# Kernel tuning notes

Hardware: AMD Instinct MI355X
Metric: run time of the kernel (lower is better)

Reference implementation:

```python
import jax, jax.numpy as jnp
import numpy as np

N = 100000       # nodes
E = 3200000      # edges (avg degree 32)
NFEAT = 512
NHID = 256
NCLASS = 64
K = 10
ALPHA = 0.1


def setup_inputs() -> dict:
    key = jax.random.key(0)
    ks = jax.random.split(key, 6)
    x = jax.random.normal(ks[0], (N, NFEAT), dtype=jnp.float32)
    edge_index = jax.random.randint(ks[1], (2, E), 0, N)
    W1 = jax.random.normal(ks[2], (NFEAT, NHID), dtype=jnp.float32) / np.float32(np.sqrt(NFEAT))
    b1 = jnp.zeros((NHID,), jnp.float32)
    W2 = jax.random.normal(ks[3], (NHID, NCLASS), dtype=jnp.float32) / np.float32(np.sqrt(NHID))
    b2 = jnp.zeros((NCLASS,), jnp.float32)
    # PPR init of the K+1 GPR coefficients: alpha*(1-alpha)^k, last = (1-alpha)^K
    kk = jnp.arange(K + 1, dtype=jnp.float32)
    temp = (ALPHA * (1.0 - ALPHA) ** kk).astype(jnp.float32)
    temp = temp.at[-1].set(np.float32((1.0 - ALPHA) ** K))
    return {"x": x, "edge_index": edge_index, "W1": W1, "b1": b1, "W2": W2, "b2": b2, "temp": temp}


def reference(x, edge_index, W1, b1, W2, b2, temp):
    # MLP (dropout is identity in eval mode)
    h = jax.nn.relu(x @ W1 + b1)          # [N, NHID]
    h = h @ W2 + b2                        # [N, NCLASS]

    # gcn_norm with self-loops: D^-1/2 (A+I) D^-1/2
    row, col = edge_index[0], edge_index[1]
    loops = jnp.arange(N, dtype=row.dtype)
    row = jnp.concatenate([row, loops])
    col = jnp.concatenate([col, loops])
    w = jnp.ones(row.shape[0], h.dtype)
    deg = jax.ops.segment_sum(w, col, num_segments=N)
    dis = jnp.where(deg > 0, jax.lax.rsqrt(deg), 0.0)
    norm = dis[row] * w * dis[col]         # [E+N]

    # K-hop GPR propagation: hidden = sum_k temp[k] * A_hat^k h
    hidden = h * temp[0]
    for k in range(K):
        h = jax.ops.segment_sum(norm[:, None] * h[row], col, num_segments=N)
        hidden = hidden + temp[k + 1] * h
    return jax.nn.log_softmax(hidden, axis=1)
```

## Files before the change

kernel.cpp:

```cpp
#include <hip/hip_runtime.h>
#include <math.h>

#define NFEAT 512
#define NHID  256
#define NCLS  64
#define KHOP  10
#define LDSTRIDE 56

typedef __attribute__((ext_vector_type(8))) short short8;
typedef __attribute__((ext_vector_type(4))) float f32x4;

__device__ __forceinline__ unsigned short f2bf(float f) {
    unsigned u = __float_as_uint(f);
    u += 0x7FFFu + ((u >> 16) & 1u);
    return (unsigned short)(u >> 16);
}
__device__ __forceinline__ float bf2f(unsigned short h) {
    return __uint_as_float((unsigned)h << 16);
}

__global__ __launch_bounds__(256) void cast_kernel(const float* __restrict__ src,
                                                   unsigned short* __restrict__ dst, long n)
{
    long i = (long)blockIdx.x * 1024 + (long)threadIdx.x * 4;
    if (i + 3 < n) {
        float4 v = *(const float4*)(src + i);
        dst[i+0] = f2bf(v.x); dst[i+1] = f2bf(v.y);
        dst[i+2] = f2bf(v.z); dst[i+3] = f2bf(v.w);
    } else {
        for (int j = 0; j < 4 && i + j < n; j++) dst[i+j] = f2bf(src[i+j]);
    }
}

__global__ __launch_bounds__(256) void castT_kernel(const float* __restrict__ src,
                                                    unsigned short* __restrict__ dst,
                                                    int K, int N)
{
    int i = blockIdx.x * 256 + threadIdx.x;
    if (i < K * N) {
        int k = i / N, n = i % N;
        dst[(long)n * K + k] = f2bf(src[i]);
    }
}

__global__ __launch_bounds__(256) void mfma_gemm1(
    const unsigned short* __restrict__ A, const unsigned short* __restrict__ BT,
    const float* __restrict__ bias, unsigned short* __restrict__ C, int M)
{
    __shared__ unsigned short As[128 * LDSTRIDE];
    __shared__ unsigned short Bs[128 * LDSTRIDE];
    const int tid = threadIdx.x;
    const int wave = tid >> 6, lane = tid & 63;
    const int quad = lane >> 4, l16 = lane & 15;
    const int wm = wave >> 1, wn = wave & 1;
    const int m0 = blockIdx.x * 128, n0 = blockIdx.y * 128;

    f32x4 acc[4][4] = {};
    const int srow = tid >> 2;
    const int schunk = (tid & 3) * 8;

    for (int k0 = 0; k0 < NFEAT; k0 += 32) {
        #pragma unroll
        for (int i = 0; i < 2; i++) {
            int r = srow + i * 64;
            int rg = m0 + r;
            short8 v = {};
            if (rg < M) v = *(const short8*)(A + (long)rg * NFEAT + k0 + schunk);
            *(short8*)(As + r * LDSTRIDE + schunk) = v;
        }
        #pragma unroll
        for (int i = 0; i < 2; i++) {
            int r = srow + i * 64;
            short8 v = *(const short8*)(BT + (long)(n0 + r) * NFEAT + k0 + schunk);
            *(short8*)(Bs + r * LDSTRIDE + schunk) = v;
        }
        __syncthreads();
        short8 af[4], bfr[4];
        #pragma unroll
        for (int mi = 0; mi < 4; mi++)
            af[mi] = *(const short8*)(As + (wm*64 + mi*16 + l16) * LDSTRIDE + quad*8);
        #pragma unroll
        for (int nj = 0; nj < 4; nj++)
            bfr[nj] = *(const short8*)(Bs + (wn*64 + nj*16 + l16) * LDSTRIDE + quad*8);
        #pragma unroll
        for (int mi = 0; mi < 4; mi++)
            #pragma unroll
            for (int nj = 0; nj < 4; nj++)
                acc[mi][nj] = __builtin_amdgcn_mfma_f32_16x16x32_bf16(af[mi], bfr[nj], acc[mi][nj], 0, 0, 0);
        __syncthreads();
    }

    #pragma unroll
    for (int mi = 0; mi < 4; mi++)
        #pragma unroll
        for (int r = 0; r < 4; r++) {
            int row = m0 + wm*64 + mi*16 + quad*4 + r;
            if (row >= M) continue;
            #pragma unroll
            for (int nj = 0; nj < 4; nj++) {
                int col = n0 + wn*64 + nj*16 + l16;
                float v = acc[mi][nj][r] + bias[col];
                C[(long)row * NHID + col] = f2bf(fmaxf(v, 0.f));
            }
        }
}

__global__ __launch_bounds__(256) void mfma_gemm2(
    const unsigned short* __restrict__ A, const unsigned short* __restrict__ BT,
    const float* __restrict__ bias, unsigned short* __restrict__ S,
    float* __restrict__ hidden, const float* __restrict__ temp,
    const float* __restrict__ dis, int M)
{
    __shared__ unsigned short As[128 * LDSTRIDE];
    __shared__ unsigned short Bs[64 * LDSTRIDE];
    const int tid = threadIdx.x;
    const int wave = tid >> 6, lane = tid & 63;
    const int quad = lane >> 4, l16 = lane & 15;
    const int m0 = blockIdx.x * 128;
    const float t0 = temp[0];

    f32x4 acc[2][4] = {};
    const int srow = tid >> 2;
    const int schunk = (tid & 3) * 8;

    for (int k0 = 0; k0 < NHID; k0 += 32) {
        #pragma unroll
        for (int i = 0; i < 2; i++) {
            int r = srow + i * 64;
            int rg = m0 + r;
            short8 v = {};
            if (rg < M) v = *(const short8*)(A + (long)rg * NHID + k0 + schunk);
            *(short8*)(As + r * LDSTRIDE + schunk) = v;
        }
        {
            short8 v = *(const short8*)(BT + (long)srow * NHID + k0 + schunk);
            *(short8*)(Bs + srow * LDSTRIDE + schunk) = v;
        }
        __syncthreads();
        short8 af[2], bfr[4];
        #pragma unroll
        for (int mi = 0; mi < 2; mi++)
            af[mi] = *(const short8*)(As + (wave*32 + mi*16 + l16) * LDSTRIDE + quad*8);
        #pragma unroll
        for (int nj = 0; nj < 4; nj++)
            bfr[nj] = *(const short8*)(Bs + (nj*16 + l16) * LDSTRIDE + quad*8);
        #pragma unroll
        for (int mi = 0; mi < 2; mi++)
            #pragma unroll
            for (int nj = 0; nj < 4; nj++)
                acc[mi][nj] = __builtin_amdgcn_mfma_f32_16x16x32_bf16(af[mi], bfr[nj], acc[mi][nj], 0, 0, 0);
        __syncthreads();
    }

    #pragma unroll
    for (int mi = 0; mi < 2; mi++)
        #pragma unroll
        for (int r = 0; r < 4; r++) {
            int row = m0 + wave*32 + mi*16 + quad*4 + r;
            if (row >= M) continue;
            float dr = dis[row];
            #pragma unroll
            for (int nj = 0; nj < 4; nj++) {
                int col = nj*16 + l16;
                float v = acc[mi][nj][r] + bias[col];
                long idx = (long)row * NCLS + col;
                S[idx] = f2bf(dr * v);
                hidden[idx] = t0 * v;
            }
        }
}

__global__ void count_kernel(const int* __restrict__ ei, int E, int* __restrict__ cnt)
{
    int e = blockIdx.x * blockDim.x + threadIdx.x;
    if (e < E) atomicAdd(&cnt[ei[E + e]], 1);
}

__global__ void dis_kernel(const int* __restrict__ cnt, float* __restrict__ dis, int Nn)
{
    int v = blockIdx.x * blockDim.x + threadIdx.x;
    if (v < Nn) dis[v] = rsqrtf((float)(cnt[v] + 1));
}

__global__ __launch_bounds__(256) void bsum_kernel(const int* __restrict__ cnt, int n,
                                                   int* __restrict__ bsum)
{
    __shared__ int ws[4];
    int i = blockIdx.x * 256 + threadIdx.x;
    int v = (i < n) ? ((cnt[i] + 7) & ~7) : 0;
    #pragma unroll
    for (int off = 1; off < 64; off <<= 1) v += __shfl_xor(v, off);
    if ((threadIdx.x & 63) == 0) ws[threadIdx.x >> 6] = v;
    __syncthreads();
    if (threadIdx.x == 0) bsum[blockIdx.x] = ws[0] + ws[1] + ws[2] + ws[3];
}

__global__ __launch_bounds__(512) void bscan_kernel(int* __restrict__ bsum, int nb)
{
    __shared__ int buf[512];
    int i = threadIdx.x;
    int v = (i < nb) ? bsum[i] : 0;
    buf[i] = v;
    __syncthreads();
    for (int off = 1; off < 512; off <<= 1) {
        int t = (i >= off) ? buf[i - off] : 0;
        __syncthreads();
        buf[i] += t;
        __syncthreads();
    }
    if (i < nb) bsum[i] = buf[i] - v;
}

__global__ __launch_bounds__(256) void pscan_kernel(const int* __restrict__ cnt, int n,
                                                    const int* __restrict__ bsum,
                                                    int* __restrict__ ptr)
{
    __shared__ int buf[256];
    int i = blockIdx.x * 256 + threadIdx.x;
    int v = (i < n) ? ((cnt[i] + 7) & ~7) : 0;
    buf[threadIdx.x] = v;
    __syncthreads();
    for (int off = 1; off < 256; off <<= 1) {
        int t = (threadIdx.x >= off) ? buf[threadIdx.x - off] : 0;
        __syncthreads();
        buf[threadIdx.x] += t;
        __syncthreads();
    }
    if (i < n) ptr[i] = bsum[blockIdx.x] + buf[threadIdx.x] - v;
    if (i == n - 1) ptr[n] = bsum[blockIdx.x] + buf[threadIdx.x];
}

__global__ void fill_kernel(const int* __restrict__ ei, int E,
                            const int* __restrict__ ptr, int* __restrict__ fill,
                            int* __restrict__ adj)
{
    int e = blockIdx.x * blockDim.x + threadIdx.x;
    if (e >= E) return;
    int r = ei[e];
    int c = ei[E + e];
    int pos = atomicAdd(&fill[c], 1);
    adj[ptr[c] + pos] = r;
}

__global__ void padfill_kernel(const int* __restrict__ cnt, const int* __restrict__ ptr,
                               int* __restrict__ adj, int Nn)
{
    int v = blockIdx.x * 256 + threadIdx.x;
    if (v >= Nn) return;
    int b = ptr[v] + cnt[v], e = ptr[v + 1];
    for (int i = b; i < e; i++) adj[i] = Nn;
}

__global__ void zdum_kernel(unsigned short* __restrict__ sA,
                            unsigned short* __restrict__ sB, int Nn)
{
    int i = threadIdx.x;
    if (i < 64) sA[(long)Nn * NCLS + i] = 0;
    else        sB[(long)Nn * NCLS + (i - 64)] = 0;
}

__global__ __launch_bounds__(256) void prop_kernel(
    const unsigned short* __restrict__ sin, unsigned short* __restrict__ sout,
    float* __restrict__ hidden,
    const int* __restrict__ ptr, const int* __restrict__ adj,
    const float* __restrict__ dis, const float* __restrict__ temp, int k, int Nn)
{
    const int wave = threadIdx.x >> 6, lane = threadIdx.x & 63;
    const int v = blockIdx.x * 4 + wave;
    if (v >= Nn) return;

    const int beg = ptr[v], end = ptr[v + 1];
    const float d = dis[v];
    float acc = bf2f(sin[v * NCLS + lane]);

    for (int e = beg; e < end; e += 8) {
        int4 u0 = *(const int4*)(adj + e);
        int4 u1 = *(const int4*)(adj + e + 4);
        float a0 = bf2f(sin[u0.x * NCLS + lane]);
        float a1 = bf2f(sin[u0.y * NCLS + lane]);
        float a2 = bf2f(sin[u0.z * NCLS + lane]);
        float a3 = bf2f(sin[u0.w * NCLS + lane]);
        float a4 = bf2f(sin[u1.x * NCLS + lane]);
        float a5 = bf2f(sin[u1.y * NCLS + lane]);
        float a6 = bf2f(sin[u1.z * NCLS + lane]);
        float a7 = bf2f(sin[u1.w * NCLS + lane]);
        acc += ((a0 + a1) + (a2 + a3)) + ((a4 + a5) + (a6 + a7));
    }

    int idx = v * NCLS + lane;
    float h = d * acc;
    hidden[idx] += temp[k + 1] * h;
    sout[idx] = f2bf(d * h);
}

__global__ __launch_bounds__(256) void lsm_kernel(const float* __restrict__ hidden,
                                                  float* __restrict__ out, int Nn)
{
    const int wave = threadIdx.x >> 6, lane = threadIdx.x & 63;
    const int v = blockIdx.x * 4 + wave;
    if (v >= Nn) return;
    float x = hidden[(long)v * NCLS + lane];
    float m = x;
    #pragma unroll
    for (int off = 32; off > 0; off >>= 1) m = fmaxf(m, __shfl_xor(m, off));
    float s = __expf(x - m);
    #pragma unroll
    for (int off = 32; off > 0; off >>= 1) s += __shfl_xor(s, off);
    out[(long)v * NCLS + lane] = x - m - logf(s);
}

extern "C" void kernel_launch(void* const* d_in, const int* in_sizes, int n_in,
                              void* d_out, int out_size, void* d_ws, size_t ws_size,
                              hipStream_t stream)
{
    const float* x    = (const float*)d_in[0];
    const int*   ei   = (const int*)  d_in[1];
    const float* W1   = (const float*)d_in[2];
    const float* b1   = (const float*)d_in[3];
    const float* W2   = (const float*)d_in[4];
    const float* b2   = (const float*)d_in[5];
    const float* temp = (const float*)d_in[6];

    const int Nn = in_sizes[0] / NFEAT;
    const int E  = in_sizes[1] / 2;

    char* ws = (char*)d_ws;
    size_t off = 0;
    auto alloc = [&](size_t bytes) { size_t o = off; off += (bytes + 255) & ~255ull; return o; };

    size_t r0 = alloc((size_t)Nn * NFEAT * 2);
    size_t hmid_off = alloc((size_t)Nn * NHID * 2);
    size_t w1t_off  = alloc((size_t)NFEAT * NHID * 2);
    size_t w2t_off  = alloc((size_t)NHID * NCLS * 2);
    size_t cnt_off  = alloc((size_t)Nn * 4);
    size_t fill_off = alloc((size_t)Nn * 4);
    size_t dis_off  = alloc((size_t)Nn * 4);
    size_t ptr_off  = alloc((size_t)(Nn + 1) * 4);
    size_t bsum_off = alloc(((size_t)Nn / 256 + 2) * 4);

    unsigned short* x_bf = (unsigned short*)(ws + r0);
    unsigned short* hmid = (unsigned short*)(ws + hmid_off);
    unsigned short* W1T  = (unsigned short*)(ws + w1t_off);
    unsigned short* W2T  = (unsigned short*)(ws + w2t_off);
    int*   cnt   = (int*)  (ws + cnt_off);
    int*   fillb = (int*)  (ws + fill_off);
    float* dis   = (float*)(ws + dis_off);
    int*   ptr   = (int*)  (ws + ptr_off);
    int*   bsum  = (int*)  (ws + bsum_off);

    size_t Epad = (size_t)E + 8ull * Nn;
    int*            adj    = (int*)           (ws + r0);
    unsigned short* sA     = (unsigned short*)(ws + r0 + Epad * 4);
    unsigned short* sB     = (unsigned short*)(ws + r0 + Epad * 4 + (size_t)(Nn + 1) * NCLS * 2);
    float*          hidden = (float*)         (ws + r0 + Epad * 4 + (size_t)(Nn + 1) * NCLS * 4);

    cast_kernel<<<(int)(((long)Nn * NFEAT + 1023) / 1024), 256, 0, stream>>>(x, x_bf, (long)Nn * NFEAT);
    castT_kernel<<<(NFEAT * NHID + 255) / 256, 256, 0, stream>>>(W1, W1T, NFEAT, NHID);
    castT_kernel<<<(NHID * NCLS + 255) / 256, 256, 0, stream>>>(W2, W2T, NHID, NCLS);

    {
        dim3 g((Nn + 127) / 128, NHID / 128);
        mfma_gemm1<<<g, 256, 0, stream>>>(x_bf, W1T, b1, hmid, Nn);
    }

    hipMemsetAsync(cnt,   0, (size_t)Nn * 4, stream);
    hipMemsetAsync(fillb, 0, (size_t)Nn * 4, stream);
    count_kernel<<<(E + 255) / 256, 256, 0, stream>>>(ei, E, cnt);
    dis_kernel<<<(Nn + 255) / 256, 256, 0, stream>>>(cnt, dis, Nn);
    int nb = (Nn + 255) / 256;
    bsum_kernel<<<nb, 256, 0, stream>>>(cnt, Nn, bsum);
    bscan_kernel<<<1, 512, 0, stream>>>(bsum, nb);
    pscan_kernel<<<nb, 256, 0, stream>>>(cnt, Nn, bsum, ptr);
    fill_kernel<<<(E + 255) / 256, 256, 0, stream>>>(ei, E, ptr, fillb, adj);
    padfill_kernel<<<(Nn + 255) / 256, 256, 0, stream>>>(cnt, ptr, adj, Nn);
    zdum_kernel<<<1, 128, 0, stream>>>(sA, sB, Nn);

    mfma_gemm2<<<(Nn + 127) / 128, 256, 0, stream>>>(hmid, W2T, b2, sA, hidden, temp, dis, Nn);

    int pg = (Nn + 3) / 4;
    for (int k = 0; k < KHOP; k++) {
        const unsigned short* sin = (k & 1) ? sB : sA;
        unsigned short*       so  = (k & 1) ? sA : sB;
        prop_kernel<<<pg, 256, 0, stream>>>(sin, so, hidden, ptr, adj, dis, temp, k, Nn);
    }

    lsm_kernel<<<pg, 256, 0, stream>>>(hidden, (float*)d_out, Nn);
}
```

Measured before the change: 1.414 ms.

## Bucket edges before CSR fill and split neighbor gathers across half-waves

CSR construction now does a two-pass bucketed scatter: edges are first grouped by 256-node destination buckets into a temporary buffer, then a per-bucket kernel fills the adjacency list, so the scattered writes stay local. The propagation kernel has each half-wave handle 8 neighbors, loading packed bf16 pairs as 32-bit words, and combines the two halves with a shuffle. Degree padding rises from 8 to 16 to match. This aims to cut random-write cost in CSR build and raise gather parallelism per node, but adds an extra pass, extra memory traffic and more padding entries for low-degree nodes.

```diff
diff --git a/kernel.cpp b/kernel.cpp
--- a/kernel.cpp
+++ b/kernel.cpp
@@ -6,6 +6,7 @@
 #define NCLS  64
 #define KHOP  10
 #define LDSTRIDE 56
+#define DEGPAD 16
 
 typedef __attribute__((ext_vector_type(8))) short short8;
 typedef __attribute__((ext_vector_type(4))) float f32x4;
@@ -18,6 +19,8 @@
 __device__ __forceinline__ float bf2f(unsigned short h) {
     return __uint_as_float((unsigned)h << 16);
 }
+__device__ __forceinline__ float bflo(unsigned w) { return __uint_as_float(w << 16); }
+__device__ __forceinline__ float bfhi(unsigned w) { return __uint_as_float(w & 0xFFFF0000u); }
 
 __global__ __launch_bounds__(256) void cast_kernel(const float* __restrict__ src,
                                                    unsigned short* __restrict__ dst, long n)
@@ -170,10 +173,14 @@
         }
 }
 
-__global__ void count_kernel(const int* __restrict__ ei, int E, int* __restrict__ cnt)
+__global__ void countA_kernel(const int* __restrict__ ei, int E,
+                              int* __restrict__ cnt, int* __restrict__ bcnt)
 {
     int e = blockIdx.x * blockDim.x + threadIdx.x;
-    if (e < E) atomicAdd(&cnt[ei[E + e]], 1);
+    if (e >= E) return;
+    int c = ei[E + e];
+    atomicAdd(&cnt[c], 1);
+    atomicAdd(&bcnt[c >> 8], 1);
 }
 
 __global__ void dis_kernel(const int* __restrict__ cnt, float* __restrict__ dis, int Nn)
@@ -187,7 +194,7 @@
 {
     __shared__ int ws[4];
     int i = blockIdx.x * 256 + threadIdx.x;
-    int v = (i < n) ? ((cnt[i] + 7) & ~7) : 0;
+    int v = (i < n) ? ((cnt[i] + DEGPAD - 1) & ~(DEGPAD - 1)) : 0;
     #pragma unroll
     for (int off = 1; off < 64; off <<= 1) v += __shfl_xor(v, off);
     if ((threadIdx.x & 63) == 0) ws[threadIdx.x >> 6] = v;
@@ -211,13 +218,31 @@
     if (i < nb) bsum[i] = buf[i] - v;
 }
 
+__global__ __launch_bounds__(512) void bscan2_kernel(const int* __restrict__ bcnt,
+                                                     int* __restrict__ boff, int nb)
+{
+    __shared__ int buf[512];
+    int i = threadIdx.x;
+    int v = (i < nb) ? bcnt[i] : 0;
+    buf[i] = v;
+    __syncthreads();
+    for (int off = 1; off < 512; off <<= 1) {
+        int t = (i >= off) ? buf[i - off] : 0;
+        __syncthreads();
+        buf[i] += t;
+        __syncthreads();
+    }
+    if (i < nb) boff[i] = buf[i] - v;
+    if (i == nb - 1) boff[nb] = buf[i];
+}
+
 __global__ __launch_bounds__(256) void pscan_kernel(const int* __restrict__ cnt, int n,
                                                     const int* __restrict__ bsum,
                                                     int* __restrict__ ptr)
 {
     __shared__ int buf[256];
     int i = blockIdx.x * 256 + threadIdx.x;
-    int v = (i < n) ? ((cnt[i] + 7) & ~7) : 0;
+    int v = (i < n) ? ((cnt[i] + DEGPAD - 1) & ~(DEGPAD - 1)) : 0;
     buf[threadIdx.x] = v;
     __syncthreads();
     for (int off = 1; off < 256; off <<= 1) {
@@ -230,16 +255,32 @@
     if (i == n - 1) ptr[n] = bsum[blockIdx.x] + buf[threadIdx.x];
 }
 
-__global__ void fill_kernel(const int* __restrict__ ei, int E,
-                            const int* __restrict__ ptr, int* __restrict__ fill,
-                            int* __restrict__ adj)
+__global__ void bucket_scatter(const int* __restrict__ ei, int E,
+                               const int* __restrict__ boff, int* __restrict__ btail,
+                               int2* __restrict__ ebuf)
 {
     int e = blockIdx.x * blockDim.x + threadIdx.x;
     if (e >= E) return;
     int r = ei[e];
     int c = ei[E + e];
-    int pos = atomicAdd(&fill[c], 1);
-    adj[ptr[c] + pos] = r;
+    int b = c >> 8;
+    int pos = atomicAdd(&btail[b], 1);
+    ebuf[boff[b] + pos] = make_int2(r, c);
+}
+
+__global__ __launch_bounds__(256) void csr_fill(const int2* __restrict__ ebuf,
+                                                const int* __restrict__ boff,
+                                                const int* __restrict__ ptr,
+                                                int* __restrict__ fill,
+                                                int* __restrict__ adj)
+{
+    int b = blockIdx.x;
+    int s = boff[b], t = boff[b + 1];
+    for (int i = s + blockIdx.y * 256 + threadIdx.x; i < t; i += gridDim.y * 256) {
+        int2 rc = ebuf[i];
+        int pos = atomicAdd(&fill[rc.y], 1);
+        adj[ptr[rc.y] + pos] = rc.x;
+    }
 }
 
 __global__ void padfill_kernel(const int* __restrict__ cnt, const int* __restrict__ ptr,
@@ -269,28 +310,52 @@
     const int v = blockIdx.x * 4 + wave;
     if (v >= Nn) return;
 
+    const int half = lane >> 5;
+    const int col2 = lane & 31;
+    const unsigned* __restrict__ s32 = (const unsigned*)sin;
+
     const int beg = ptr[v], end = ptr[v + 1];
     const float d = dis[v];
-    float acc = bf2f(sin[v * NCLS + lane]);
-
-    for (int e = beg; e < end; e += 8) {
-        int4 u0 = *(const int4*)(adj + e);
-        int4 u1 = *(const int4*)(adj + e + 4);
-        float a0 = bf2f(sin[u0.x * NCLS + lane]);
-        float a1 = bf2f(sin[u0.y * NCLS + lane]);
-        float a2 = bf2f(sin[u0.z * NCLS + lane]);
-        float a3 = bf2f(sin[u0.w * NCLS + lane]);
-        float a4 = bf2f(sin[u1.x * NCLS + lane]);
-        float a5 = bf2f(sin[u1.y * NCLS + lane]);
-        float a6 = bf2f(sin[u1.z * NCLS + lane]);
-        float a7 = bf2f(sin[u1.w * NCLS + lane]);
-        acc += ((a0 + a1) + (a2 + a3)) + ((a4 + a5) + (a6 + a7));
-    }
-
-    int idx = v * NCLS + lane;
-    float h = d * acc;
-    hidden[idx] += temp[k + 1] * h;
-    sout[idx] = f2bf(d * h);
+
+    float ax = 0.f, ay = 0.f;
+    {
+        unsigned w = s32[(long)v * 32 + col2];
+        if (half == 0) { ax = bflo(w); ay = bfhi(w); }
+    }
+
+    for (int e = beg; e < end; e += 16) {
+        int base = e + (half << 3);
+        int4 u0 = *(const int4*)(adj + base);
+        int4 u1 = *(const int4*)(adj + base + 4);
+        unsigned w0 = s32[(long)u0.x * 32 + col2];
+        unsigned w1 = s32[(long)u0.y * 32 + col2];
+        unsigned w2 = s32[(long)u0.z * 32 + col2];
+        unsigned w3 = s32[(long)u0.w * 32 + col2];
+        unsigned w4 = s32[(long)u1.x * 32 + col2];
+        unsigned w5 = s32[(long)u1.y * 32 + col2];
+        unsigned w6 = s32[(long)u1.z * 32 + col2];
+        unsigned w7 = s32[(long)u1.w * 32 + col2];
+        ax += ((bflo(w0) + bflo(w1)) + (bflo(w2) + bflo(w3)))
+            + ((bflo(w4) + bflo(w5)) + (bflo(w6) + bflo(w7)));
+        ay += ((bfhi(w0) + bfhi(w1)) + (bfhi(w2) + bfhi(w3)))
+            + ((bfhi(w4) + bfhi(w5)) + (bfhi(w6) + bfhi(w7)));
+    }
+
+    ax += __shfl_xor(ax, 32);
+    ay += __shfl_xor(ay, 32);
+
+    if (half == 0) {
+        int col = col2 * 2;
+        long idx = (long)v * NCLS + col;
+        float h0 = d * ax, h1 = d * ay;
+        float tk = temp[k + 1];
+        float2* hp = (float2*)(hidden + idx);
+        float2 hv = *hp;
+        hv.x += tk * h0; hv.y += tk * h1;
+        *hp = hv;
+        unsigned pack = (unsigned)f2bf(d * h0) | ((unsigned)f2bf(d * h1) << 16);
+        *(unsigned*)(sout + idx) = pack;
+    }
 }
 
 __global__ __launch_bounds__(256) void lsm_kernel(const float* __restrict__ hidden,
@@ -323,6 +388,7 @@
 
     const int Nn = in_sizes[0] / NFEAT;
     const int E  = in_sizes[1] / 2;
+    const int nbk = ((Nn - 1) >> 8) + 1;
 
     char* ws = (char*)d_ws;
     size_t off = 0;
@@ -337,6 +403,9 @@
     size_t dis_off  = alloc((size_t)Nn * 4);
     size_t ptr_off  = alloc((size_t)(Nn + 1) * 4);
     size_t bsum_off = alloc(((size_t)Nn / 256 + 2) * 4);
+    size_t bcnt_off = alloc((size_t)(nbk + 1) * 4);
+    size_t boff_off = alloc((size_t)(nbk + 1) * 4);
+    size_t btail_off= alloc((size_t)(nbk + 1) * 4);
 
     unsigned short* x_bf = (unsigned short*)(ws + r0);
     unsigned short* hmid = (unsigned short*)(ws + hmid_off);
@@ -347,12 +416,19 @@
     float* dis   = (float*)(ws + dis_off);
     int*   ptr   = (int*)  (ws + ptr_off);
     int*   bsum  = (int*)  (ws + bsum_off);
-
-    size_t Epad = (size_t)E + 8ull * Nn;
+    int*   bcnt  = (int*)  (ws + bcnt_off);
+    int*   boff  = (int*)  (ws + boff_off);
+    int*   btail = (int*)  (ws + btail_off);
+
+    size_t Epad  = (size_t)E + (size_t)DEGPAD * Nn;
+    size_t adjB  = Epad * 4;
+    size_t sBsz  = (size_t)(Nn + 1) * NCLS * 2;
+    size_t hidB  = (size_t)Nn * NCLS * 4;
     int*            adj    = (int*)           (ws + r0);
-    unsigned short* sA     = (unsigned short*)(ws + r0 + Epad * 4);
-    unsigned short* sB     = (unsigned short*)(ws + r0 + Epad * 4 + (size_t)(Nn + 1) * NCLS * 2);
-    float*          hidden = (float*)         (ws + r0 + Epad * 4 + (size_t)(Nn + 1) * NCLS * 4);
+    unsigned short* sA     = (unsigned short*)(ws + r0 + adjB);
+    unsigned short* sB     = (unsigned short*)(ws + r0 + adjB + sBsz);
+    float*          hidden = (float*)         (ws + r0 + adjB + 2 * sBsz);
+    int2*           ebuf   = (int2*)          (ws + r0 + adjB + 2 * sBsz + hidB);
 
     cast_kernel<<<(int)(((long)Nn * NFEAT + 1023) / 1024), 256, 0, stream>>>(x, x_bf, (long)Nn * NFEAT);
     castT_kernel<<<(NFEAT * NHID + 255) / 256, 256, 0, stream>>>(W1, W1T, NFEAT, NHID);
@@ -365,13 +441,20 @@
 
     hipMemsetAsync(cnt,   0, (size_t)Nn * 4, stream);
     hipMemsetAsync(fillb, 0, (size_t)Nn * 4, stream);
-    count_kernel<<<(E + 255) / 256, 256, 0, stream>>>(ei, E, cnt);
+    hipMemsetAsync(bcnt,  0, (size_t)(nbk + 1) * 4, stream);
+    hipMemsetAsync(btail, 0, (size_t)(nbk + 1) * 4, stream);
+    countA_kernel<<<(E + 255) / 256, 256, 0, stream>>>(ei, E, cnt, bcnt);
     dis_kernel<<<(Nn + 255) / 256, 256, 0, stream>>>(cnt, dis, Nn);
     int nb = (Nn + 255) / 256;
     bsum_kernel<<<nb, 256, 0, stream>>>(cnt, Nn, bsum);
     bscan_kernel<<<1, 512, 0, stream>>>(bsum, nb);
     pscan_kernel<<<nb, 256, 0, stream>>>(cnt, Nn, bsum, ptr);
-    fill_kernel<<<(E + 255) / 256, 256, 0, stream>>>(ei, E, ptr, fillb, adj);
+    bscan2_kernel<<<1, 512, 0, stream>>>(bcnt, boff, nbk);
+    bucket_scatter<<<(E + 255) / 256, 256, 0, stream>>>(ei, E, boff, btail, ebuf);
+    {
+        dim3 g(nbk, 8);
+        csr_fill<<<g, 256, 0, stream>>>(ebuf, boff, ptr, fillb, adj);
+    }
     padfill_kernel<<<(Nn + 255) / 256, 256, 0, stream>>>(cnt, ptr, adj, Nn);
     zdum_kernel<<<1, 128, 0, stream>>>(sA, sB, Nn);
 
```

Measured after the change: 3.438 ms. +143.2%, slower.
